# Optimization experiments

Measured on AMD Instinct MI355X. Metric: run time of the kernel, lower is better.

Reference implementation:

```python
import jax, jax.numpy as jnp
import numpy as np

QMAX = 32767.0   # 2**15 - 1
QMIN = -32768.0  # -2**15


def setup_inputs() -> dict:
    key = jax.random.key(0)
    k_x, k_w0, k_w1, k_s, k_b = jax.random.split(key, 5)
    N, Cin, Cout = 8192, 4096, 4096
    x = jax.random.normal(k_x, (N, Cin, 1, 1), dtype=jnp.float32)
    # Fake-quantized INT8 weights: build a fp32 weight, split into dual int8 planes
    # the same way prepare_from_weight does, so w0/w1 hold integer values in [-128,127].
    W = jax.random.normal(k_w0, (Cout, Cin), dtype=jnp.float32) * 0.02
    max_abs = jnp.maximum(jnp.max(jnp.abs(W), axis=1), 1e-8)
    s0 = max_abs / 127.0
    w0 = jnp.clip(jnp.round(W / s0[:, None]), -128.0, 127.0)
    R = W - s0[:, None] * w0
    max_abs_R = jnp.max(jnp.abs(R), axis=1)
    s1 = jnp.where(max_abs_R > 1e-3, max_abs_R / 127.0, 0.0)
    w1 = jnp.where((s1 > 0)[:, None],
                   jnp.clip(jnp.round(R / jnp.where(s1 > 0, s1, 1.0)[:, None]), -128.0, 127.0),
                   0.0)
    bias = jax.random.normal(k_b, (Cout,), dtype=jnp.float32) * 0.01
    return {"x": x, "w0": w0, "w1": w1, "s0": s0, "s1": s1, "bias": bias}


def reference(x, w0, w1, s0, s1, bias):
    N, Cin, H, W_ = x.shape  # H == W_ == 1
    x2d = x.reshape(N, Cin)
    # INT16 activation fake-quant with softplus-smoothed amax
    amax = jnp.max(jnp.abs(x2d), axis=1, keepdims=True)          # [N,1]
    scale_x = jax.nn.softplus(amax) / QMAX                       # [N,1]
    xq = jnp.clip(jnp.round(x2d / scale_x), QMIN, QMAX)          # [N,Cin]
    # dual 1x1 convs == two GEMMs: [N,Cin] x [Cin,Cout]
    y0 = jnp.einsum('nc,oc->no', xq, w0)
    y1 = jnp.einsum('nc,oc->no', xq, w1)
    y = (y0 * s0[None, :] + y1 * s1[None, :]) * scale_x + bias[None, :]
    return y.reshape(N, -1, 1, 1)
```

## Files before the change

kernel.cpp:

```cpp
#include <hip/hip_runtime.h>
#include <hip/hip_fp16.h>

#define N_ROWS 8192
#define K_DIM  4096
#define M_DIM  4096
#define NT     (K_DIM / 64)
#define HT_MAX (4 * NT)

typedef __attribute__((ext_vector_type(8))) _Float16 half8;
typedef __attribute__((ext_vector_type(4))) _Float16 half4v;
typedef __attribute__((ext_vector_type(4))) float    f32x4;

__global__ __launch_bounds__(256) void quant_kernel(
    const float* __restrict__ x, _Float16* __restrict__ xq, float* __restrict__ sx)
{
    const int t    = threadIdx.x;
    const int lane = t & 63;
    const int row  = blockIdx.x * 4 + (t >> 6);
    const float4* xr4 = (const float4*)(x + (size_t)row * K_DIM);

    float4 v[16];
    float am = 0.0f;
#pragma unroll
    for (int j = 0; j < 16; ++j) {
        v[j] = xr4[j * 64 + lane];
        am = fmaxf(am, fmaxf(fmaxf(fabsf(v[j].x), fabsf(v[j].y)),
                             fmaxf(fabsf(v[j].z), fabsf(v[j].w))));
    }
#pragma unroll
    for (int off = 32; off; off >>= 1)
        am = fmaxf(am, __shfl_xor(am, off, 64));

    const float sp    = (am > 20.0f) ? am : log1pf(expf(am));
    const float scale = sp * (1.0f / 32767.0f);
    const float inv   = 32767.0f / sp;
    if (lane == 0) sx[row] = scale;

    half4v* out4 = (half4v*)(xq + (size_t)row * K_DIM);
#pragma unroll
    for (int j = 0; j < 16; ++j) {
        half4v h;
        h[0] = (_Float16)fminf(fmaxf(rintf(v[j].x * inv), -32768.0f), 32767.0f);
        h[1] = (_Float16)fminf(fmaxf(rintf(v[j].y * inv), -32768.0f), 32767.0f);
        h[2] = (_Float16)fminf(fmaxf(rintf(v[j].z * inv), -32768.0f), 32767.0f);
        h[3] = (_Float16)fminf(fmaxf(rintf(v[j].w * inv), -32768.0f), 32767.0f);
        out4[j * 64 + lane] = h;
    }
}

__global__ __launch_bounds__(256) void fold_kernel(
    const float* __restrict__ w0, const float* __restrict__ w1,
    const float* __restrict__ s0, const float* __restrict__ s1,
    _Float16* __restrict__ wp)
{
    const size_t gid = (size_t)blockIdx.x * 256 + threadIdx.x;
    const int    o   = (int)(gid >> 10);
    const float  a = s0[o], b = s1[o];

    const float4 u = ((const float4*)w0)[gid];
    const float4 v = ((const float4*)w1)[gid];
    half4v h;
    h[0] = (_Float16)(a * u.x + b * v.x);
    h[1] = (_Float16)(a * u.y + b * v.y);
    h[2] = (_Float16)(a * u.z + b * v.z);
    h[3] = (_Float16)(a * u.w + b * v.w);
    ((half4v*)wp)[gid] = h;
}

__device__ inline void async_load16(const void* g, void* l)
{
    __builtin_amdgcn_global_load_lds(
        (const __attribute__((address_space(1))) void*)g,
        (__attribute__((address_space(3))) void*)l, 16, 0, 0);
}

#define PHASE(BUF, KS, MH, RDB, PP, KP, HT, GATE)                             \
    {                                                                         \
        if (RDB) {                                                            \
            _Pragma("unroll")                                                 \
            for (int j = 0; j < 4; ++j) {                                     \
                const int r = wn * 64 + j * 16 + fr;                          \
                const int c = fg ^ ((r >> 1) & 3);                            \
                bf[KP][j] =                                                   \
                    *(const half8*)&Bs[BUF][(KS) * 8192 + r * 32 + c * 8];    \
            }                                                                 \
        }                                                                     \
        _Pragma("unroll")                                                     \
        for (int i = 0; i < 4; ++i) {                                         \
            const int r = wm * 128 + (MH) * 64 + i * 16 + fr;                 \
            const int c = fg ^ ((r >> 1) & 3);                                \
            af[PP][i] =                                                       \
                *(const half8*)&As[BUF][(KS) * 8192 + r * 32 + c * 8];        \
        }                                                                     \
        stage(HT);                                                            \
        __builtin_amdgcn_s_barrier();                                         \
        asm volatile("" ::: "memory");                                        \
        asm volatile("s_waitcnt lgkmcnt(0)" ::: "memory");                    \
        __builtin_amdgcn_sched_barrier(0);                                    \
        __builtin_amdgcn_s_setprio(1);                                        \
        _Pragma("unroll")                                                     \
        for (int i = 0; i < 4; ++i)                                           \
            _Pragma("unroll")                                                 \
            for (int j = 0; j < 4; ++j)                                       \
                acc[(MH) * 4 + i][j] = __builtin_amdgcn_mfma_f32_16x16x32_f16(\
                    af[PP][i], bf[KP][j], acc[(MH) * 4 + i][j], 0, 0, 0);     \
        __builtin_amdgcn_s_setprio(0);                                        \
        if ((GATE) == 0)                                                      \
            asm volatile("s_waitcnt vmcnt(0)" ::: "memory");                  \
        else if ((GATE) > 0)                                                  \
            asm volatile("s_waitcnt vmcnt(4)" ::: "memory");                  \
        __builtin_amdgcn_s_barrier();                                         \
        asm volatile("" ::: "memory");                                        \
    }

__global__ __launch_bounds__(512, 2) void gemm_kernel(
    const _Float16* __restrict__ A,
    const _Float16* __restrict__ B,
    const float* __restrict__ sx,
    const float* __restrict__ bias,
    float* __restrict__ out)
{
    __shared__ __align__(16) _Float16 As[2][16384];
    __shared__ __align__(16) _Float16 Bs[2][16384];

    const int t    = threadIdx.x;
    const int lane = t & 63;
    const int wave = t >> 6;
    const int wm   = wave >> 2;
    const int wn   = wave & 3;

    const int b2  = (blockIdx.x & 7) * 64 + (blockIdx.x >> 3);
    const int sup = b2 >> 6;
    const int loc = b2 & 63;
    const int tm  = (sup & 1) * 8 + (loc & 7);
    const int tn  = (sup >> 1) * 8 + (loc >> 3);
    const int n0  = tn * 256;
    const int o0  = tm * 256;

    const int fr = lane & 15;
    const int fg = lane >> 4;

    f32x4 acc[8][4] = {};

    auto stage = [&](int ht_) {
        if (ht_ >= HT_MAX) return;
        const int Tt  = ht_ >> 2;
        const int prt = ht_ & 3;
        const int ks  = prt >> 1;
        const int kof = Tt * 64 + ks * 32;
        _Float16* lbase = ((prt & 1) ? &Bs[Tt & 1][0] : &As[Tt & 1][0]) + ks * 8192;
        const _Float16* gbase = (prt & 1) ? B + (size_t)o0 * K_DIM
                                          : A + (size_t)n0 * K_DIM;
#pragma unroll
        for (int l = 0; l < 2; ++l) {
            const int s  = l * 512 + t;
            const int r  = s >> 2;
            const int pc = s & 3;
            const int c  = pc ^ ((r >> 1) & 3);
            async_load16(gbase + (size_t)r * K_DIM + kof + c * 8,
                         lbase + r * 32 + pc * 8);
        }
    };

#pragma unroll
    for (int h = 0; h < 6; ++h) stage(h);
    asm volatile("s_waitcnt vmcnt(4)" ::: "memory");
    __builtin_amdgcn_s_barrier();
    asm volatile("" ::: "memory");

    half8 af[2][4], bf[2][4];
    int ht = 6;
#pragma unroll 1
    for (int it = 0; it < NT / 2; ++it) {
        const int g = (it == NT / 2 - 1) ? 0 : 4;
        PHASE(0,  0, 0, 1,  0, 0, ht + 0, -1)
        PHASE(0,  0, 1, 0,  1, 0, ht + 1, -1)
        PHASE(0,  1, 0, 1,  0, 1, ht + 2, -1)
        PHASE(0,  1, 1, 0,  1, 1, ht + 3, g)
        PHASE(1,  0, 0, 1,  0, 0, ht + 4, -1)
        PHASE(1,  0, 1, 0,  1, 0, ht + 5, -1)
        PHASE(1,  1, 0, 1,  0, 1, ht + 6, -1)
        PHASE(1,  1, 1, 0,  1, 1, ht + 7, g)
        ht += 8;
    }

    float bs[4];
#pragma unroll
    for (int j = 0; j < 4; ++j)
        bs[j] = bias[o0 + wn * 64 + j * 16 + fr];
#pragma unroll
    for (int i = 0; i < 8; ++i) {
        const int nb = n0 + wm * 128 + i * 16 + fg * 4;
#pragma unroll
        for (int r = 0; r < 4; ++r) {
            const float s = sx[nb + r];
            float* orow = out + (size_t)(nb + r) * M_DIM;
#pragma unroll
            for (int j = 0; j < 4; ++j)
                orow[o0 + wn * 64 + j * 16 + fr] = acc[i][j][r] * s + bs[j];
        }
    }
}

extern "C" void kernel_launch(void* const* d_in, const int* in_sizes, int n_in,
                              void* d_out, int out_size, void* d_ws, size_t ws_size,
                              hipStream_t stream)
{
    const float* x    = (const float*)d_in[0];
    const float* w0   = (const float*)d_in[1];
    const float* w1   = (const float*)d_in[2];
    const float* s0   = (const float*)d_in[3];
    const float* s1   = (const float*)d_in[4];
    const float* bias = (const float*)d_in[5];
    float* out = (float*)d_out;

    char* ws = (char*)d_ws;
    _Float16* xq = (_Float16*)ws;
    _Float16* wp = (_Float16*)(ws + (size_t)N_ROWS * K_DIM * 2);
    float*    sx = (float*)(ws + (size_t)N_ROWS * K_DIM * 2
                               + (size_t)M_DIM * K_DIM * 2);

    quant_kernel<<<N_ROWS / 4, 256, 0, stream>>>(x, xq, sx);
    fold_kernel<<<(M_DIM * K_DIM) / (256 * 4), 256, 0, stream>>>(w0, w1, s0, s1, wp);

    gemm_kernel<<<(N_ROWS / 256) * (M_DIM / 256), 512, 0, stream>>>(
        xq, wp, sx, bias, out);
}
```

Measured before the change: 579.6 us.

## Prefetch next phase LDS fragments during current MFMA phase

Restructures the GEMM main loop so each phase issues LDS reads for the next phase's A/B fragments before computing MFMAs on the fragments loaded in the previous phase. A prologue loads the first fragments, and the lgkmcnt waits become partial so only the older reads must complete. Global-load vmcnt gating moves to the start of phases with a tighter count, and a final drain is added after the loop. The aim is to hide LDS read latency behind matrix math. In exchange there is more register pressure from double-buffered fragments and more delicate wait-count correctness.

```diff
diff --git a/kernel.cpp b/kernel.cpp
--- a/kernel.cpp
+++ b/kernel.cpp
@@ -74,41 +74,42 @@
         (__attribute__((address_space(3))) void*)l, 16, 0, 0);
 }
 
-#define PHASE(BUF, KS, MH, RDB, PP, KP, HT, GATE)                             \
+#define PHASE(GATE, BN, KN, MN, RDBN, KP, MP, HT)                             \
     {                                                                         \
-        if (RDB) {                                                            \
+        if (GATE)                                                             \
+            asm volatile("s_waitcnt vmcnt(2)" ::: "memory");                  \
+        if (RDBN) {                                                           \
             _Pragma("unroll")                                                 \
             for (int j = 0; j < 4; ++j) {                                     \
                 const int r = wn * 64 + j * 16 + fr;                          \
                 const int c = fg ^ ((r >> 1) & 3);                            \
-                bf[KP][j] =                                                   \
-                    *(const half8*)&Bs[BUF][(KS) * 8192 + r * 32 + c * 8];    \
+                bf[KN][j] =                                                   \
+                    *(const half8*)&Bs[BN][(KN) * 8192 + r * 32 + c * 8];     \
             }                                                                 \
         }                                                                     \
         _Pragma("unroll")                                                     \
         for (int i = 0; i < 4; ++i) {                                         \
-            const int r = wm * 128 + (MH) * 64 + i * 16 + fr;                 \
+            const int r = wm * 128 + (MN) * 64 + i * 16 + fr;                 \
             const int c = fg ^ ((r >> 1) & 3);                                \
-            af[PP][i] =                                                       \
-                *(const half8*)&As[BUF][(KS) * 8192 + r * 32 + c * 8];        \
+            af[MN][i] =                                                       \
+                *(const half8*)&As[BN][(KN) * 8192 + r * 32 + c * 8];         \
         }                                                                     \
         stage(HT);                                                            \
+        asm volatile("" ::: "memory");                                        \
         __builtin_amdgcn_s_barrier();                                         \
         asm volatile("" ::: "memory");                                        \
-        asm volatile("s_waitcnt lgkmcnt(0)" ::: "memory");                    \
+        asm volatile("s_waitcnt lgkmcnt(%0)" :: "i"((RDBN) ? 8 : 4)           \
+                     : "memory");                                             \
         __builtin_amdgcn_sched_barrier(0);                                    \
         __builtin_amdgcn_s_setprio(1);                                        \
         _Pragma("unroll")                                                     \
         for (int i = 0; i < 4; ++i)                                           \
             _Pragma("unroll")                                                 \
             for (int j = 0; j < 4; ++j)                                       \
-                acc[(MH) * 4 + i][j] = __builtin_amdgcn_mfma_f32_16x16x32_f16(\
-                    af[PP][i], bf[KP][j], acc[(MH) * 4 + i][j], 0, 0, 0);     \
+                acc[(MP) * 4 + i][j] = __builtin_amdgcn_mfma_f32_16x16x32_f16(\
+                    af[MP][i], bf[KP][j], acc[(MP) * 4 + i][j], 0, 0, 0);     \
         __builtin_amdgcn_s_setprio(0);                                        \
-        if ((GATE) == 0)                                                      \
-            asm volatile("s_waitcnt vmcnt(0)" ::: "memory");                  \
-        else if ((GATE) > 0)                                                  \
-            asm volatile("s_waitcnt vmcnt(4)" ::: "memory");                  \
+        asm volatile("" ::: "memory");                                        \
         __builtin_amdgcn_s_barrier();                                         \
         asm volatile("" ::: "memory");                                        \
     }
@@ -164,25 +165,38 @@
 
 #pragma unroll
     for (int h = 0; h < 6; ++h) stage(h);
-    asm volatile("s_waitcnt vmcnt(4)" ::: "memory");
+    asm volatile("s_waitcnt vmcnt(8)" ::: "memory");
     __builtin_amdgcn_s_barrier();
     asm volatile("" ::: "memory");
 
     half8 af[2][4], bf[2][4];
+#pragma unroll
+    for (int j = 0; j < 4; ++j) {
+        const int r = wn * 64 + j * 16 + fr;
+        const int c = fg ^ ((r >> 1) & 3);
+        bf[0][j] = *(const half8*)&Bs[0][r * 32 + c * 8];
+    }
+#pragma unroll
+    for (int i = 0; i < 4; ++i) {
+        const int r = wm * 128 + i * 16 + fr;
+        const int c = fg ^ ((r >> 1) & 3);
+        af[0][i] = *(const half8*)&As[0][r * 32 + c * 8];
+    }
+
     int ht = 6;
 #pragma unroll 1
     for (int it = 0; it < NT / 2; ++it) {
-        const int g = (it == NT / 2 - 1) ? 0 : 4;
-        PHASE(0,  0, 0, 1,  0, 0, ht + 0, -1)
-        PHASE(0,  0, 1, 0,  1, 0, ht + 1, -1)
-        PHASE(0,  1, 0, 1,  0, 1, ht + 2, -1)
-        PHASE(0,  1, 1, 0,  1, 1, ht + 3, g)
-        PHASE(1,  0, 0, 1,  0, 0, ht + 4, -1)
-        PHASE(1,  0, 1, 0,  1, 0, ht + 5, -1)
-        PHASE(1,  1, 0, 1,  0, 1, ht + 6, -1)
-        PHASE(1,  1, 1, 0,  1, 1, ht + 7, g)
+        PHASE(0,   0, 0, 1, 0,   0, 0, ht + 0)
+        PHASE(1,   0, 1, 0, 1,   0, 1, ht + 1)
+        PHASE(0,   0, 1, 1, 0,   1, 0, ht + 2)
+        PHASE(1,   1, 0, 0, 1,   1, 1, ht + 3)
+        PHASE(0,   1, 0, 1, 0,   0, 0, ht + 4)
+        PHASE(1,   1, 1, 0, 1,   0, 1, ht + 5)
+        PHASE(0,   1, 1, 1, 0,   1, 0, ht + 6)
+        PHASE(1,   0, 0, 0, 1,   1, 1, ht + 7)
         ht += 8;
     }
+    asm volatile("s_waitcnt vmcnt(0)" ::: "memory");
 
     float bs[4];
 #pragma unroll
```

New measurement: 581.2 us. No clear change (+0.3%).

## Replace direct global-to-LDS async loads with register-staged prefetch pipeline

Applied to the files above, without the earlier changes.

Drops the global_load_lds async copies. Tiles now load into registers two phases ahead and are written to swizzled LDS a phase later, under a new schedule that removes the vmcnt gates. This lets the swizzle be applied on the LDS write side and puts data movement on the ordinary VGPR path. The cost is extra VGPRs for the staged values and implicit vmcnt waits before the LDS stores, which may lower occupancy or stall the MFMA stream.

```diff
diff --git a/kernel.cpp b/kernel.cpp
--- a/kernel.cpp
+++ b/kernel.cpp
@@ -67,34 +67,57 @@
     ((half4v*)wp)[gid] = h;
 }
 
-__device__ inline void async_load16(const void* g, void* l)
-{
-    __builtin_amdgcn_global_load_lds(
-        (const __attribute__((address_space(1))) void*)g,
-        (__attribute__((address_space(3))) void*)l, 16, 0, 0);
-}
-
-#define PHASE(BUF, KS, MH, RDB, PP, KP, HT, GATE)                             \
+
+#define PH(P)                                                                 \
     {                                                                         \
-        if (RDB) {                                                            \
+        constexpr int BUF = (P) >> 2;                                         \
+        constexpr int KS  = ((P) >> 1) & 1;                                   \
+        constexpr int MH  = (P) & 1;                                          \
+        constexpr int PAR = ((P) + 3) & 1;                                    \
+        constexpr int WPRT = ((P) + 3) & 3;                                   \
+        constexpr int WISB = WPRT & 1;                                        \
+        constexpr int WKS  = WPRT >> 1;                                       \
+        constexpr int WBUF = (((P) + 3) >> 2) & 1;                            \
+        constexpr int GPRT = ((P) + 5) & 3;                                   \
+        constexpr int GISB = GPRT & 1;                                        \
+        constexpr int GKS  = GPRT >> 1;                                       \
+        constexpr int GTOF = ((P) + 5) >> 2;                                  \
+        if (MH == 0) {                                                        \
             _Pragma("unroll")                                                 \
             for (int j = 0; j < 4; ++j) {                                     \
                 const int r = wn * 64 + j * 16 + fr;                          \
                 const int c = fg ^ ((r >> 1) & 3);                            \
-                bf[KP][j] =                                                   \
-                    *(const half8*)&Bs[BUF][(KS) * 8192 + r * 32 + c * 8];    \
+                bf[j] = *(const half8*)&Bs[BUF][KS * 8192 + r * 32 + c * 8];  \
             }                                                                 \
         }                                                                     \
         _Pragma("unroll")                                                     \
         for (int i = 0; i < 4; ++i) {                                         \
-            const int r = wm * 128 + (MH) * 64 + i * 16 + fr;                 \
+            const int r = wm * 128 + MH * 64 + i * 16 + fr;                   \
             const int c = fg ^ ((r >> 1) & 3);                                \
-            af[PP][i] =                                                       \
-                *(const half8*)&As[BUF][(KS) * 8192 + r * 32 + c * 8];        \
-        }                                                                     \
-        stage(HT);                                                            \
+            af[i] = *(const half8*)&As[BUF][KS * 8192 + r * 32 + c * 8];      \
+        }                                                                     \
+        if (it * 8 + (P) + 3 < HT_MAX) {                                      \
+            _Float16* lb = (WISB ? &Bs[WBUF][0] : &As[WBUF][0]) + WKS * 8192; \
+            _Pragma("unroll")                                                 \
+            for (int l = 0; l < 2; ++l) {                                     \
+                const int sl = l * 512 + t, r = sl >> 2, pc = sl & 3;         \
+                const int c = pc ^ ((r >> 1) & 3);                            \
+                *(int4*)&lb[r * 32 + c * 8] = gr[PAR][l];                     \
+            }                                                                 \
+        }                                                                     \
+        if (it * 8 + (P) + 5 < HT_MAX) {                                      \
+            const _Float16* gb = GISB ? B + (size_t)o0 * K_DIM                \
+                                      : A + (size_t)n0 * K_DIM;               \
+            const int kof = (it * 2 + GTOF) * 64 + GKS * 32;                  \
+            _Pragma("unroll")                                                 \
+            for (int l = 0; l < 2; ++l) {                                     \
+                const int sl = l * 512 + t, r = sl >> 2, pc = sl & 3;         \
+                gr[PAR][l] =                                                  \
+                    *(const int4*)&gb[(size_t)r * K_DIM + kof + pc * 8];      \
+            }                                                                 \
+        }                                                                     \
+        asm volatile("" ::: "memory");                                        \
         __builtin_amdgcn_s_barrier();                                         \
-        asm volatile("" ::: "memory");                                        \
         asm volatile("s_waitcnt lgkmcnt(0)" ::: "memory");                    \
         __builtin_amdgcn_sched_barrier(0);                                    \
         __builtin_amdgcn_s_setprio(1);                                        \
@@ -102,13 +125,10 @@
         for (int i = 0; i < 4; ++i)                                           \
             _Pragma("unroll")                                                 \
             for (int j = 0; j < 4; ++j)                                       \
-                acc[(MH) * 4 + i][j] = __builtin_amdgcn_mfma_f32_16x16x32_f16(\
-                    af[PP][i], bf[KP][j], acc[(MH) * 4 + i][j], 0, 0, 0);     \
+                acc[MH * 4 + i][j] = __builtin_amdgcn_mfma_f32_16x16x32_f16(  \
+                    af[i], bf[j], acc[MH * 4 + i][j], 0, 0, 0);               \
         __builtin_amdgcn_s_setprio(0);                                        \
-        if ((GATE) == 0)                                                      \
-            asm volatile("s_waitcnt vmcnt(0)" ::: "memory");                  \
-        else if ((GATE) > 0)                                                  \
-            asm volatile("s_waitcnt vmcnt(4)" ::: "memory");                  \
+        asm volatile("" ::: "memory");                                        \
         __builtin_amdgcn_s_barrier();                                         \
         asm volatile("" ::: "memory");                                        \
     }
@@ -141,47 +161,38 @@
     const int fg = lane >> 4;
 
     f32x4 acc[8][4] = {};
-
-    auto stage = [&](int ht_) {
-        if (ht_ >= HT_MAX) return;
-        const int Tt  = ht_ >> 2;
-        const int prt = ht_ & 3;
+    int4  gr[2][2];
+
+#pragma unroll
+    for (int s = 0; s < 3; ++s) {
+        const int prt = s;
         const int ks  = prt >> 1;
-        const int kof = Tt * 64 + ks * 32;
-        _Float16* lbase = ((prt & 1) ? &Bs[Tt & 1][0] : &As[Tt & 1][0]) + ks * 8192;
-        const _Float16* gbase = (prt & 1) ? B + (size_t)o0 * K_DIM
-                                          : A + (size_t)n0 * K_DIM;
+        const _Float16* gb = (prt & 1) ? B + (size_t)o0 * K_DIM
+                                       : A + (size_t)n0 * K_DIM;
+        _Float16* lb = ((prt & 1) ? &Bs[0][0] : &As[0][0]) + ks * 8192;
+        const int kof = ks * 32;
 #pragma unroll
         for (int l = 0; l < 2; ++l) {
-            const int s  = l * 512 + t;
-            const int r  = s >> 2;
-            const int pc = s & 3;
-            const int c  = pc ^ ((r >> 1) & 3);
-            async_load16(gbase + (size_t)r * K_DIM + kof + c * 8,
-                         lbase + r * 32 + pc * 8);
+            const int sl = l * 512 + t, r = sl >> 2, pc = sl & 3;
+            const int c = pc ^ ((r >> 1) & 3);
+            int4 v = *(const int4*)&gb[(size_t)r * K_DIM + kof + pc * 8];
+            *(int4*)&lb[r * 32 + c * 8] = v;
         }
-    };
-
-#pragma unroll
-    for (int h = 0; h < 6; ++h) stage(h);
-    asm volatile("s_waitcnt vmcnt(4)" ::: "memory");
+    }
+#pragma unroll
+    for (int l = 0; l < 2; ++l) {
+        const int sl = l * 512 + t, r = sl >> 2, pc = sl & 3;
+        gr[1][l] = *(const int4*)&B[(size_t)(o0 + r) * K_DIM + 32 + pc * 8];
+        gr[0][l] = *(const int4*)&A[(size_t)(n0 + r) * K_DIM + 64 + pc * 8];
+    }
+    asm volatile("s_waitcnt lgkmcnt(0)" ::: "memory");
     __builtin_amdgcn_s_barrier();
     asm volatile("" ::: "memory");
 
-    half8 af[2][4], bf[2][4];
-    int ht = 6;
+    half8 af[4], bf[4];
 #pragma unroll 1
     for (int it = 0; it < NT / 2; ++it) {
-        const int g = (it == NT / 2 - 1) ? 0 : 4;
-        PHASE(0,  0, 0, 1,  0, 0, ht + 0, -1)
-        PHASE(0,  0, 1, 0,  1, 0, ht + 1, -1)
-        PHASE(0,  1, 0, 1,  0, 1, ht + 2, -1)
-        PHASE(0,  1, 1, 0,  1, 1, ht + 3, g)
-        PHASE(1,  0, 0, 1,  0, 0, ht + 4, -1)
-        PHASE(1,  0, 1, 0,  1, 0, ht + 5, -1)
-        PHASE(1,  1, 0, 1,  0, 1, ht + 6, -1)
-        PHASE(1,  1, 1, 0,  1, 1, ht + 7, g)
-        ht += 8;
+        PH(0) PH(1) PH(2) PH(3) PH(4) PH(5) PH(6) PH(7)
     }
 
     float bs[4];
```

New measurement: 765.7 us. 32.1% more time.
